# Optimization experiments

Measured on AMD Instinct MI355X. Metric: run time of the kernel, lower is better.

Reference implementation:

```python
import jax, jax.numpy as jnp
import numpy as np

B, T, C = 2, 2048, 1024
NH, HD = 16, 64  # n_head, head_dim (qk == vo)


def setup_inputs() -> dict:
    key = jax.random.key(0)
    ks = jax.random.split(key, 5)
    scale = 1.0 / np.sqrt(C)
    return {
        "x": jax.random.normal(ks[0], (B, T, C), dtype=jnp.float32),
        "Wq": jax.random.normal(ks[1], (C, C), dtype=jnp.float32) * scale,
        "Wk": jax.random.normal(ks[2], (C, C), dtype=jnp.float32) * scale,
        "Wv": jax.random.normal(ks[3], (C, C), dtype=jnp.float32) * scale,
        "Wo": jax.random.normal(ks[4], (C, C), dtype=jnp.float32) * scale,
    }


def reference(x, Wq, Wk, Wv, Wo):
    # torch Linear: y = x @ W.T (weights stored [out, in])
    q = (x @ Wq.T).reshape(B, T, NH, HD).transpose(0, 2, 1, 3)  # [B,H,T,D]
    k = (x @ Wk.T).reshape(B, T, NH, HD).transpose(0, 2, 1, 3)
    v = (x @ Wv.T).reshape(B, T, NH, HD).transpose(0, 2, 1, 3)
    att = jnp.einsum("bhqd,bhkd->bhqk", q, k) * (1.0 / np.sqrt(HD))
    causal = jnp.tril(jnp.ones((T, T), dtype=bool))
    att = jnp.where(causal[None, None], att, -jnp.inf)
    att = jax.nn.softmax(att, axis=-1)
    y = jnp.einsum("bhqk,bhkd->bhqd", att, v)  # [B,H,T,D]
    y = y.transpose(0, 2, 1, 3).reshape(B, T, NH * HD)
    return y @ Wo.T  # dropout p=0 -> identity
```

## Files before the change

kernel.cpp:

```cpp
#include <hip/hip_runtime.h>
#include <hip/hip_bf16.h>
#include <cstdint>
#include <cstddef>
#include <cmath>

#define B_  2
#define T_  2048
#define C_  1024
#define NH_ 16
#define HD_ 64

typedef __bf16 bf16;
typedef bf16  bf16x8 __attribute__((ext_vector_type(8)));
typedef bf16  bf16x4 __attribute__((ext_vector_type(4)));
typedef float f32x4  __attribute__((ext_vector_type(4)));

#define MFMA16(a, b, c) __builtin_amdgcn_mfma_f32_16x16x32_bf16((a), (b), (c), 0, 0, 0)

__device__ __forceinline__ void gld_lds16(const bf16* g, bf16* lds_base_uniform) {
    __builtin_amdgcn_global_load_lds(
        (const __attribute__((address_space(1))) uint32_t*)g,
        (__attribute__((address_space(3))) uint32_t*)lds_base_uniform,
        16, 0, 0);
}

__global__ __launch_bounds__(256) void cast_f32_bf16(const float* __restrict__ in,
                                                     bf16* __restrict__ out, int n4) {
    int i = blockIdx.x * 256 + threadIdx.x;
    if (i < n4) {
        float4 v = ((const float4*)in)[i];
        bf16x4 o = { (bf16)v.x, (bf16)v.y, (bf16)v.z, (bf16)v.w };
        ((bf16x4*)out)[i] = o;
    }
}

__global__ __launch_bounds__(256) void cast_weights(const float* __restrict__ Wq,
                                                    const float* __restrict__ Wk,
                                                    const float* __restrict__ Wv,
                                                    const float* __restrict__ Wo,
                                                    bf16* __restrict__ Wqk,
                                                    bf16* __restrict__ Wvb,
                                                    bf16* __restrict__ Wob) {
    const float C1 = 0.1803368801111f;
    const int i = blockIdx.x * 256 + threadIdx.x;
    const int nw4 = C_ * C_ / 4;
    float4 q = ((const float4*)Wq)[i];
    float4 k = ((const float4*)Wk)[i];
    float4 v = ((const float4*)Wv)[i];
    float4 o = ((const float4*)Wo)[i];
    ((bf16x4*)Wqk)[i]       = bf16x4{ (bf16)(q.x * C1), (bf16)(q.y * C1),
                                      (bf16)(q.z * C1), (bf16)(q.w * C1) };
    ((bf16x4*)Wqk)[nw4 + i] = bf16x4{ (bf16)k.x, (bf16)k.y, (bf16)k.z, (bf16)k.w };
    ((bf16x4*)Wvb)[i]       = bf16x4{ (bf16)v.x, (bf16)v.y, (bf16)v.z, (bf16)v.w };
    ((bf16x4*)Wob)[i]       = bf16x4{ (bf16)o.x, (bf16)o.y, (bf16)o.z, (bf16)o.w };
}

__device__ __forceinline__ void gemm_tile(bf16* As, bf16* Bs,
                                          const bf16* __restrict__ A,
                                          const bf16* __restrict__ W,
                                          bf16* __restrict__ Y,
                                          int N, int K, int m0, int n0) {
    const int tid  = threadIdx.x;
    const int lane = tid & 63;
    const int w    = tid >> 6;
    const int ml   = lane & 15;
    const int quad = lane >> 4;
    const int wm   = (w >> 1) * 64;
    const int wn   = (w & 1) * 64;
    const int sr   = lane >> 2;
    const int sc   = lane & 3;

    f32x4 acc[4][4] = {};

    for (int k0 = 0; k0 < K; k0 += 32) {
        __syncthreads();
#pragma unroll
        for (int ei = 0; ei < 2; ++ei) {
            const int e = w * 2 + ei;
            gld_lds16(A + (size_t)(m0 + e * 16 + sr) * K + k0 + sc * 8, &As[e * 512]);
            gld_lds16(W + (size_t)(n0 + e * 16 + sr) * K + k0 + sc * 8, &Bs[e * 512]);
        }
        __builtin_amdgcn_s_waitcnt(0);
        __syncthreads();

        bf16x8 af[4], bfr[4];
#pragma unroll
        for (int t = 0; t < 4; ++t) {
            af[t]  = *(const bf16x8*)&As[(wm + t * 16 + ml) * 32 + quad * 8];
            bfr[t] = *(const bf16x8*)&Bs[(wn + t * 16 + ml) * 32 + quad * 8];
        }
#pragma unroll
        for (int mt = 0; mt < 4; ++mt)
#pragma unroll
            for (int nt = 0; nt < 4; ++nt)
                acc[mt][nt] = MFMA16(af[mt], bfr[nt], acc[mt][nt]);
    }

#pragma unroll
    for (int mt = 0; mt < 4; ++mt)
#pragma unroll
        for (int nt = 0; nt < 4; ++nt)
#pragma unroll
            for (int r = 0; r < 4; ++r) {
                const int row = m0 + wm + mt * 16 + quad * 4 + r;
                const int col = n0 + wn + nt * 16 + ml;
                Y[(size_t)row * N + col] = (bf16)acc[mt][nt][r];
            }
}

__global__ __launch_bounds__(256) void proj_fused(const bf16* __restrict__ xb,
                                                  const bf16* __restrict__ Wqk,
                                                  const bf16* __restrict__ Wvb,
                                                  bf16* __restrict__ QKb,
                                                  bf16* __restrict__ VtT) {
    __shared__ __align__(16) bf16 As[128 * 32];
    __shared__ __align__(16) bf16 Bs[128 * 32];
    const int bid = blockIdx.x;
    if (bid < 512) {
        gemm_tile(As, Bs, xb, Wqk, QKb, 2048, 1024, (bid >> 4) * 128, (bid & 15) * 128);
    } else {
        const int b2 = bid - 512;
        gemm_tile(As, Bs, Wvb, xb, VtT, 4096, 1024, (b2 >> 5) * 128, (b2 & 31) * 128);
    }
}

__global__ __launch_bounds__(256) void gemm_wo(const bf16* __restrict__ A,
                                               const bf16* __restrict__ W,
                                               float* __restrict__ Y) {
    __shared__ __align__(16) bf16 As[64 * 32];
    __shared__ __align__(16) bf16 Bs[128 * 32];
    const int tid  = threadIdx.x;
    const int lane = tid & 63;
    const int w    = tid >> 6;
    const int ml   = lane & 15;
    const int quad = lane >> 4;
    const int wm   = (w >> 1) * 32;
    const int wn   = (w & 1) * 64;
    const int m0   = blockIdx.y * 64;
    const int n0   = blockIdx.x * 128;
    const int sr   = lane >> 2;
    const int sc   = lane & 3;

    f32x4 acc[2][4] = {};

    for (int k0 = 0; k0 < 1024; k0 += 32) {
        __syncthreads();
        gld_lds16(A + (size_t)(m0 + w * 16 + sr) * 1024 + k0 + sc * 8, &As[w * 512]);
#pragma unroll
        for (int ei = 0; ei < 2; ++ei) {
            const int e = w * 2 + ei;
            gld_lds16(W + (size_t)(n0 + e * 16 + sr) * 1024 + k0 + sc * 8, &Bs[e * 512]);
        }
        __builtin_amdgcn_s_waitcnt(0);
        __syncthreads();

        bf16x8 af[2], bfr[4];
#pragma unroll
        for (int t = 0; t < 2; ++t)
            af[t] = *(const bf16x8*)&As[(wm + t * 16 + ml) * 32 + quad * 8];
#pragma unroll
        for (int t = 0; t < 4; ++t)
            bfr[t] = *(const bf16x8*)&Bs[(wn + t * 16 + ml) * 32 + quad * 8];
#pragma unroll
        for (int mt = 0; mt < 2; ++mt)
#pragma unroll
            for (int nt = 0; nt < 4; ++nt)
                acc[mt][nt] = MFMA16(af[mt], bfr[nt], acc[mt][nt]);
    }

#pragma unroll
    for (int mt = 0; mt < 2; ++mt)
#pragma unroll
        for (int nt = 0; nt < 4; ++nt)
#pragma unroll
            for (int r = 0; r < 4; ++r) {
                const int row = m0 + wm + mt * 16 + quad * 4 + r;
                const int col = n0 + wn + nt * 16 + ml;
                Y[(size_t)row * 1024 + col] = acc[mt][nt][r];
            }
}

__global__ __launch_bounds__(256, 4) void attn_mfma(const bf16* __restrict__ QKb,
                                                    const bf16* __restrict__ VtT,
                                                    bf16* __restrict__ Pbuf,
                                                    float* __restrict__ Lbuf) {
    const int bid  = blockIdx.x;
    const int hb   = bid & 31;
    const int s    = 79 - (bid >> 5);
    int qt, chunk;
    if (s < 8)       { qt = s;                   chunk = 0; }
    else if (s < 24) { qt = 8  + ((s - 8) >> 1); chunk = (s - 8) & 1; }
    else if (s < 48) { qt = 16 + (s - 24) / 3;   chunk = (s - 24) % 3; }
    else             { qt = 24 + ((s - 48) >> 2); chunk = (s - 48) & 3; }
    const int h = hb >> 1, b = hb & 1;

    const int tid  = threadIdx.x;
    const int lane = tid & 63;
    const int w    = tid >> 6;
    const int ml   = lane & 15;
    const int quad = lane >> 4;

    __shared__ __align__(16) bf16 Ks[2][4096];
    __shared__ __align__(16) bf16 Vs[4096];
    __shared__ __align__(16) bf16 Ps[4][16 * 72];

    const bf16* Qbase = QKb + (size_t)b * T_ * 2048 + (size_t)h * HD_;
    const bf16* Kbase = Qbase + 1024;
    const bf16* Vbase = VtT + (size_t)h * HD_ * 4096 + (size_t)b * T_;

    const int qrow = qt * 64 + w * 16 + ml;
    bf16x8 qf[2];
#pragma unroll
    for (int ks = 0; ks < 2; ++ks)
        qf[ks] = *(const bf16x8*)(Qbase + (size_t)qrow * 2048 + ks * 32 + quad * 8);

    f32x4 o_acc[4] = {};
    f32x4 l_acc = {};
    bf16x8 onesf;
#pragma unroll
    for (int j = 0; j < 8; ++j) onesf[j] = (bf16)1.0f;

    const int sr = lane >> 2, sc = lane & 3;
    bf16* ps = &Ps[w][0];

    const int ktbase  = chunk * 8;
    const int nrounds = min(8, qt + 1 - ktbase);

    auto stageK = [&](int ktg, int buf) {
        const int k0 = ktg * 64;
#pragma unroll
        for (int ei = 0; ei < 2; ++ei) {
            const int e = w * 2 + ei;
            const int r = (e & 3) * 16 + sr;
            const int ch = (e >> 2) * 32 + sc * 8;
            gld_lds16(Kbase + (size_t)(k0 + r) * 2048 + ch, &Ks[buf][e * 512]);
        }
    };
    auto stageV = [&](int ktg) {
        const int k0 = ktg * 64;
#pragma unroll
        for (int ei = 0; ei < 2; ++ei) {
            const int e = w * 2 + ei;
            const int r = (e & 3) * 16 + sr;
            const int ch = (e >> 2) * 32 + sc * 8;
            gld_lds16(Vbase + (size_t)r * 4096 + k0 + ch, &Vs[e * 512]);
        }
    };

    auto phase1 = [&](int cur, int ktg) {
        const int k0 = ktg * 64;
#pragma unroll
        for (int nt = 0; nt < 4; ++nt) {
            f32x4 sacc = {};
#pragma unroll
            for (int ks = 0; ks < 2; ++ks) {
                bf16x8 kf = *(const bf16x8*)&Ks[cur][ks * 2048 + (nt * 16 + ml) * 32 + quad * 8];
                sacc = MFMA16(qf[ks], kf, sacc);
            }
            const int kg = k0 + nt * 16 + ml;
#pragma unroll
            for (int r = 0; r < 4; ++r) {
                float arg = sacc[r];
                if (ktg == qt) {
                    const int qg = qt * 64 + w * 16 + quad * 4 + r;
                    if (kg > qg) arg = -1e30f;
                }
                ps[(quad * 4 + r) * 72 + nt * 16 + ml] = (bf16)exp2f(arg);
            }
        }
    };

    auto phase2 = [&]() {
#pragma unroll
        for (int ks = 0; ks < 2; ++ks) {
            bf16x8 pf = *(const bf16x8*)&ps[ml * 72 + ks * 32 + quad * 8];
            l_acc = MFMA16(pf, onesf, l_acc);
#pragma unroll
            for (int nt = 0; nt < 4; ++nt) {
                bf16x8 vf = *(const bf16x8*)&Vs[ks * 2048 + (nt * 16 + ml) * 32 + quad * 8];
                o_acc[nt] = MFMA16(pf, vf, o_acc[nt]);
            }
        }
    };

    stageK(ktbase, 0);

    for (int j = 0; j < nrounds; ++j) {
        const int cur = j & 1;
        const int ktg = ktbase + j;

        asm volatile("s_barrier" ::: "memory");
        stageV(ktg);
        if (j + 1 < nrounds) {
            stageK(ktg + 1, cur ^ 1);
            asm volatile("s_waitcnt vmcnt(4)" ::: "memory");
            asm volatile("s_barrier" ::: "memory");
            phase1(cur, ktg);
            asm volatile("s_waitcnt vmcnt(2)" ::: "memory");
            asm volatile("s_barrier" ::: "memory");
            phase2();
        } else {
            asm volatile("s_waitcnt vmcnt(2)" ::: "memory");
            asm volatile("s_barrier" ::: "memory");
            phase1(cur, ktg);
            asm volatile("s_waitcnt vmcnt(0)" ::: "memory");
            asm volatile("s_barrier" ::: "memory");
            phase2();
        }
    }

    const int slotIdx = hb * 80 + s;
    bf16* pb = Pbuf + (size_t)slotIdx * 4096;
#pragma unroll
    for (int r = 0; r < 4; ++r) {
        const int prow = w * 16 + quad * 4 + r;
#pragma unroll
        for (int nt = 0; nt < 4; ++nt)
            pb[prow * 64 + nt * 16 + ml] = (bf16)o_acc[nt][r];
        if (ml == 0)
            Lbuf[slotIdx * 64 + prow] = l_acc[r];
    }
}

__global__ __launch_bounds__(256) void attn_merge(const bf16* __restrict__ Pbuf,
                                                  const float* __restrict__ Lbuf,
                                                  bf16* __restrict__ Ab) {
    const int gid = blockIdx.x;
    const int qt  = gid >> 5;
    const int hb  = gid & 31;
    const int h = hb >> 1, b = hb & 1;
    int s0;
    if (qt < 8)       s0 = qt;
    else if (qt < 16) s0 = 8 + (qt - 8) * 2;
    else if (qt < 24) s0 = 24 + (qt - 16) * 3;
    else              s0 = 48 + (qt - 24) * 4;
    const int nch = (qt + 8) >> 3;

    const int tid = threadIdx.x;
    const int row = tid >> 2;
    const int cg  = (tid & 3) * 16;

    float acc[16] = {};
    float lsum = 0.f;
    for (int c = 0; c < nch; ++c) {
        const int slotIdx = hb * 80 + s0 + c;
        lsum += Lbuf[slotIdx * 64 + row];
        const bf16* pb = Pbuf + (size_t)slotIdx * 4096 + row * 64 + cg;
        bf16x8 v0 = *(const bf16x8*)pb;
        bf16x8 v1 = *(const bf16x8*)(pb + 8);
#pragma unroll
        for (int j = 0; j < 8; ++j) { acc[j] += (float)v0[j]; acc[8 + j] += (float)v1[j]; }
    }
    const float rcl = 1.0f / lsum;
    bf16x8 o0, o1;
#pragma unroll
    for (int j = 0; j < 8; ++j) { o0[j] = (bf16)(acc[j] * rcl); o1[j] = (bf16)(acc[8 + j] * rcl); }
    bf16* dst = Ab + (size_t)(b * T_ + qt * 64 + row) * 1024 + h * 64 + cg;
    *(bf16x8*)dst = o0;
    *(bf16x8*)(dst + 8) = o1;
}

extern "C" void kernel_launch(void* const* d_in, const int* in_sizes, int n_in,
                              void* d_out, int out_size, void* d_ws, size_t ws_size,
                              hipStream_t stream) {
    const float* x  = (const float*)d_in[0];
    const float* Wq = (const float*)d_in[1];
    const float* Wk = (const float*)d_in[2];
    const float* Wv = (const float*)d_in[3];
    const float* Wo = (const float*)d_in[4];
    float* out = (float*)d_out;

    const size_t n_x = (size_t)B_ * T_ * C_;
    const size_t n_w = (size_t)C_ * C_;

    bf16* xb   = (bf16*)d_ws;
    bf16* Wqk  = xb + n_x;
    bf16* Wvb  = Wqk + 2 * n_w;
    bf16* Wob  = Wvb + n_w;
    bf16* QKb  = Wob + n_w;
    bf16* VtT  = QKb + 2 * n_x;
    bf16* Ab   = VtT + n_x;
    bf16* Pbuf = Ab + n_x;
    float* Lbuf = (float*)(Pbuf + (size_t)2560 * 4096);

    cast_f32_bf16<<<(int)(n_x / 4 / 256), 256, 0, stream>>>(x, xb, (int)(n_x / 4));
    cast_weights<<<(int)(n_w / 4 / 256), 256, 0, stream>>>(Wq, Wk, Wv, Wo, Wqk, Wvb, Wob);

    proj_fused<<<768, 256, 0, stream>>>(xb, Wqk, Wvb, QKb, VtT);

    attn_mfma<<<2560, 256, 0, stream>>>(QKb, VtT, Pbuf, Lbuf);
    attn_merge<<<1024, 256, 0, stream>>>(Pbuf, Lbuf, Ab);

    gemm_wo<<<dim3(1024 / 128, 4096 / 64), 256, 0, stream>>>(Ab, Wob, out);
}
```

Before: 186.4 us.

## Double-buffer LDS in projection and output GEMMs, merge cast kernels

Both GEMM kernels now use two LDS buffers. The next K-slice is fetched with global_load_lds while the current one feeds the MFMAs, with partial vmcnt waits and raw s_barrier replacing full waitcnt(0) plus syncthreads. The aim is to hide global load latency behind compute. The two fp32-to-bf16 cast kernels are merged into a single launch to save one kernel launch. LDS use doubles, which may reduce occupancy, and the hand-written vmcnt counts must match the number of loads issued per stage.

```diff
diff --git a/kernel.cpp b/kernel.cpp
--- a/kernel.cpp
+++ b/kernel.cpp
@@ -24,35 +24,34 @@
         16, 0, 0);
 }
 
-__global__ __launch_bounds__(256) void cast_f32_bf16(const float* __restrict__ in,
-                                                     bf16* __restrict__ out, int n4) {
-    int i = blockIdx.x * 256 + threadIdx.x;
-    if (i < n4) {
-        float4 v = ((const float4*)in)[i];
-        bf16x4 o = { (bf16)v.x, (bf16)v.y, (bf16)v.z, (bf16)v.w };
-        ((bf16x4*)out)[i] = o;
-    }
-}
-
-__global__ __launch_bounds__(256) void cast_weights(const float* __restrict__ Wq,
-                                                    const float* __restrict__ Wk,
-                                                    const float* __restrict__ Wv,
-                                                    const float* __restrict__ Wo,
-                                                    bf16* __restrict__ Wqk,
-                                                    bf16* __restrict__ Wvb,
-                                                    bf16* __restrict__ Wob) {
-    const float C1 = 0.1803368801111f;
-    const int i = blockIdx.x * 256 + threadIdx.x;
-    const int nw4 = C_ * C_ / 4;
-    float4 q = ((const float4*)Wq)[i];
-    float4 k = ((const float4*)Wk)[i];
-    float4 v = ((const float4*)Wv)[i];
-    float4 o = ((const float4*)Wo)[i];
-    ((bf16x4*)Wqk)[i]       = bf16x4{ (bf16)(q.x * C1), (bf16)(q.y * C1),
-                                      (bf16)(q.z * C1), (bf16)(q.w * C1) };
-    ((bf16x4*)Wqk)[nw4 + i] = bf16x4{ (bf16)k.x, (bf16)k.y, (bf16)k.z, (bf16)k.w };
-    ((bf16x4*)Wvb)[i]       = bf16x4{ (bf16)v.x, (bf16)v.y, (bf16)v.z, (bf16)v.w };
-    ((bf16x4*)Wob)[i]       = bf16x4{ (bf16)o.x, (bf16)o.y, (bf16)o.z, (bf16)o.w };
+__global__ __launch_bounds__(256) void cast_all(const float* __restrict__ x,
+                                                const float* __restrict__ Wq,
+                                                const float* __restrict__ Wk,
+                                                const float* __restrict__ Wv,
+                                                const float* __restrict__ Wo,
+                                                bf16* __restrict__ xb,
+                                                bf16* __restrict__ Wqk,
+                                                bf16* __restrict__ Wvb,
+                                                bf16* __restrict__ Wob) {
+    const int bid = blockIdx.x;
+    if (bid < 4096) {
+        const int i = bid * 256 + threadIdx.x;
+        float4 v = ((const float4*)x)[i];
+        ((bf16x4*)xb)[i] = bf16x4{ (bf16)v.x, (bf16)v.y, (bf16)v.z, (bf16)v.w };
+    } else {
+        const float C1 = 0.1803368801111f;
+        const int i = (bid - 4096) * 256 + threadIdx.x;
+        const int nw4 = C_ * C_ / 4;
+        float4 q = ((const float4*)Wq)[i];
+        float4 k = ((const float4*)Wk)[i];
+        float4 v = ((const float4*)Wv)[i];
+        float4 o = ((const float4*)Wo)[i];
+        ((bf16x4*)Wqk)[i]       = bf16x4{ (bf16)(q.x * C1), (bf16)(q.y * C1),
+                                          (bf16)(q.z * C1), (bf16)(q.w * C1) };
+        ((bf16x4*)Wqk)[nw4 + i] = bf16x4{ (bf16)k.x, (bf16)k.y, (bf16)k.z, (bf16)k.w };
+        ((bf16x4*)Wvb)[i]       = bf16x4{ (bf16)v.x, (bf16)v.y, (bf16)v.z, (bf16)v.w };
+        ((bf16x4*)Wob)[i]       = bf16x4{ (bf16)o.x, (bf16)o.y, (bf16)o.z, (bf16)o.w };
+    }
 }
 
 __device__ __forceinline__ void gemm_tile(bf16* As, bf16* Bs,
@@ -72,22 +71,36 @@
 
     f32x4 acc[4][4] = {};
 
-    for (int k0 = 0; k0 < K; k0 += 32) {
-        __syncthreads();
+    auto stage = [&](int k0, int buf) {
 #pragma unroll
         for (int ei = 0; ei < 2; ++ei) {
             const int e = w * 2 + ei;
-            gld_lds16(A + (size_t)(m0 + e * 16 + sr) * K + k0 + sc * 8, &As[e * 512]);
-            gld_lds16(W + (size_t)(n0 + e * 16 + sr) * K + k0 + sc * 8, &Bs[e * 512]);
-        }
-        __builtin_amdgcn_s_waitcnt(0);
-        __syncthreads();
+            gld_lds16(A + (size_t)(m0 + e * 16 + sr) * K + k0 + sc * 8,
+                      &As[buf * 4096 + e * 512]);
+            gld_lds16(W + (size_t)(n0 + e * 16 + sr) * K + k0 + sc * 8,
+                      &Bs[buf * 4096 + e * 512]);
+        }
+    };
+
+    stage(0, 0);
+    const int niter = K / 32;
+
+    for (int it = 0; it < niter; ++it) {
+        const int cur = it & 1;
+        asm volatile("s_barrier" ::: "memory");
+        if (it + 1 < niter) {
+            stage((it + 1) * 32, cur ^ 1);
+            asm volatile("s_waitcnt vmcnt(4)" ::: "memory");
+        } else {
+            asm volatile("s_waitcnt vmcnt(0)" ::: "memory");
+        }
+        asm volatile("s_barrier" ::: "memory");
 
         bf16x8 af[4], bfr[4];
 #pragma unroll
         for (int t = 0; t < 4; ++t) {
-            af[t]  = *(const bf16x8*)&As[(wm + t * 16 + ml) * 32 + quad * 8];
-            bfr[t] = *(const bf16x8*)&Bs[(wn + t * 16 + ml) * 32 + quad * 8];
+            af[t]  = *(const bf16x8*)&As[cur * 4096 + (wm + t * 16 + ml) * 32 + quad * 8];
+            bfr[t] = *(const bf16x8*)&Bs[cur * 4096 + (wn + t * 16 + ml) * 32 + quad * 8];
         }
 #pragma unroll
         for (int mt = 0; mt < 4; ++mt)
@@ -113,8 +126,8 @@
                                                   const bf16* __restrict__ Wvb,
                                                   bf16* __restrict__ QKb,
                                                   bf16* __restrict__ VtT) {
-    __shared__ __align__(16) bf16 As[128 * 32];
-    __shared__ __align__(16) bf16 Bs[128 * 32];
+    __shared__ __align__(16) bf16 As[2 * 4096];
+    __shared__ __align__(16) bf16 Bs[2 * 4096];
     const int bid = blockIdx.x;
     if (bid < 512) {
         gemm_tile(As, Bs, xb, Wqk, QKb, 2048, 1024, (bid >> 4) * 128, (bid & 15) * 128);
@@ -127,8 +140,8 @@
 __global__ __launch_bounds__(256) void gemm_wo(const bf16* __restrict__ A,
                                                const bf16* __restrict__ W,
                                                float* __restrict__ Y) {
-    __shared__ __align__(16) bf16 As[64 * 32];
-    __shared__ __align__(16) bf16 Bs[128 * 32];
+    __shared__ __align__(16) bf16 As[2 * 2048];
+    __shared__ __align__(16) bf16 Bs[2 * 4096];
     const int tid  = threadIdx.x;
     const int lane = tid & 63;
     const int w    = tid >> 6;
@@ -143,24 +156,37 @@
 
     f32x4 acc[2][4] = {};
 
-    for (int k0 = 0; k0 < 1024; k0 += 32) {
-        __syncthreads();
-        gld_lds16(A + (size_t)(m0 + w * 16 + sr) * 1024 + k0 + sc * 8, &As[w * 512]);
+    auto stage = [&](int k0, int buf) {
+        gld_lds16(A + (size_t)(m0 + w * 16 + sr) * 1024 + k0 + sc * 8,
+                  &As[buf * 2048 + w * 512]);
 #pragma unroll
         for (int ei = 0; ei < 2; ++ei) {
             const int e = w * 2 + ei;
-            gld_lds16(W + (size_t)(n0 + e * 16 + sr) * 1024 + k0 + sc * 8, &Bs[e * 512]);
-        }
-        __builtin_amdgcn_s_waitcnt(0);
-        __syncthreads();
+            gld_lds16(W + (size_t)(n0 + e * 16 + sr) * 1024 + k0 + sc * 8,
+                      &Bs[buf * 4096 + e * 512]);
+        }
+    };
+
+    stage(0, 0);
+
+    for (int it = 0; it < 32; ++it) {
+        const int cur = it & 1;
+        asm volatile("s_barrier" ::: "memory");
+        if (it + 1 < 32) {
+            stage((it + 1) * 32, cur ^ 1);
+            asm volatile("s_waitcnt vmcnt(3)" ::: "memory");
+        } else {
+            asm volatile("s_waitcnt vmcnt(0)" ::: "memory");
+        }
+        asm volatile("s_barrier" ::: "memory");
 
         bf16x8 af[2], bfr[4];
 #pragma unroll
         for (int t = 0; t < 2; ++t)
-            af[t] = *(const bf16x8*)&As[(wm + t * 16 + ml) * 32 + quad * 8];
+            af[t] = *(const bf16x8*)&As[cur * 2048 + (wm + t * 16 + ml) * 32 + quad * 8];
 #pragma unroll
         for (int t = 0; t < 4; ++t)
-            bfr[t] = *(const bf16x8*)&Bs[(wn + t * 16 + ml) * 32 + quad * 8];
+            bfr[t] = *(const bf16x8*)&Bs[cur * 4096 + (wn + t * 16 + ml) * 32 + quad * 8];
 #pragma unroll
         for (int mt = 0; mt < 2; ++mt)
 #pragma unroll
@@ -383,8 +409,7 @@
     bf16* Pbuf = Ab + n_x;
     float* Lbuf = (float*)(Pbuf + (size_t)2560 * 4096);
 
-    cast_f32_bf16<<<(int)(n_x / 4 / 256), 256, 0, stream>>>(x, xb, (int)(n_x / 4));
-    cast_weights<<<(int)(n_w / 4 / 256), 256, 0, stream>>>(Wq, Wk, Wv, Wo, Wqk, Wvb, Wob);
+    cast_all<<<5120, 256, 0, stream>>>(x, Wq, Wk, Wv, Wo, xb, Wqk, Wvb, Wob);
 
     proj_fused<<<768, 256, 0, stream>>>(xb, Wqk, Wvb, QKb, VtT);
 
```

After: 194.5 us. 1.04x slower.
